# Kernel tuning notes

Hardware: AMD Instinct MI355X
Metric: run time of the kernel (lower is better)

## Reference

```python
import jax, jax.numpy as jnp
import numpy as np

_GAUSS_2D = np.array([[1.,4.,6.,4.,1.],[4.,16.,24.,16.,4.],[6.,24.,36.,24.,6.],[4.,16.,24.,16.,4.],[1.,4.,6.,4.,1.]], dtype=np.float32) / 256.0
_GX = np.array([[2.,0.,-2.],[4.,0.,-4.],[2.,0.,-2.]], dtype=np.float32)
_GY = np.array([[2.,4.,2.],[0.,0.,0.],[-2.,-4.,-2.]], dtype=np.float32)


def _conv_gauss(img, kernel):
    # reflect-pad by 2 on H,W (matches F.pad(img,(2,2,2,2),'reflect')), then depthwise VALID conv
    img = jnp.pad(img, ((0, 0), (0, 0), (2, 2), (2, 2)), mode='reflect')
    return jax.lax.conv_general_dilated(
        img, kernel, window_strides=(1, 1), padding='VALID',
        feature_group_count=img.shape[1],
        dimension_numbers=('NCHW', 'OIHW', 'NCHW'))


def _downsample(x):
    return x[:, :, ::2, ::2]


def _upsample(x, gk):
    # zero-interleave: x at even (h,w) indices, zeros elsewhere, then smooth with 4*gauss
    B, C, H, W = x.shape
    up = jnp.zeros((B, C, 2 * H, 2 * W), dtype=x.dtype).at[:, :, ::2, ::2].set(x)
    return _conv_gauss(up, 4.0 * gk)


def _laplacian_pyramid(img, gk, max_levels=3):
    C = img.shape[1]
    gx = jnp.broadcast_to(jnp.asarray(_GX)[None, None], (C, 1, 3, 3))
    gy = jnp.broadcast_to(jnp.asarray(_GY)[None, None], (C, 1, 3, 3))
    current = img
    pyr = []
    for _ in range(max_levels):
        filtered = _conv_gauss(current, gk)
        down = _downsample(filtered)
        up = _upsample(down, gk)
        diff = current - up
        # note: pad=2 with 3x3 kernel -> output is (H+2, W+2), faithful to source
        miniloss = jnp.abs(_conv_gauss(diff, gx)) + jnp.abs(_conv_gauss(diff, gy))
        pyr.append(miniloss)
        current = down
    return pyr


def setup_inputs() -> dict:
    key = jax.random.key(0)
    k1, k2 = jax.random.split(key)
    B, C, H, W = 16, 3, 512, 512
    inp = jax.random.normal(k1, (B, C, H, W), dtype=jnp.float32)
    tgt = jax.random.normal(k2, (B, C, H, W), dtype=jnp.float32)
    gk = jnp.broadcast_to(jnp.asarray(_GAUSS_2D)[None, None], (C, 1, 5, 5)).astype(jnp.float32)
    return {'input': inp, 'target': tgt, 'gauss_kernel': gk}


def reference(input, target, gauss_kernel):
    max_levels = 3
    pyr_in = _laplacian_pyramid(input, gauss_kernel, max_levels)
    pyr_tg = _laplacian_pyramid(target, gauss_kernel, max_levels)
    loss = jnp.asarray(0.0, dtype=input.dtype)
    for a, b in zip(pyr_in, pyr_tg):
        loss = loss + jnp.mean(jnp.abs(a - b))  # l1_loss, mean reduction
    return loss
```

## Files before the change

kernel.cpp:

```cpp
#include <hip/hip_runtime.h>


#define NCH 48

__device__ __forceinline__ int refl(int p, int n) {
  return p < 0 ? -p : (p >= n ? 2 * n - 2 - p : p);
}

__global__ __launch_bounds__(256) void down_kernel(
    const float* __restrict__ src_a, const float* __restrict__ src_b,
    float* __restrict__ dst_a, float* __restrict__ dst_b, int H)
{
  const int W = H, W2 = W >> 1;
  const int bx = blockIdx.x, by = blockIdx.y;
  const int z = blockIdx.z;
  const int ch = (z >= NCH) ? z - NCH : z;
  const float* src = ((z >= NCH) ? src_b : src_a) + (size_t)ch * H * W;
  float* dst = ((z >= NCH) ? dst_b : dst_a) + (size_t)ch * W2 * W2;
  const int tid = threadIdx.x;

  __shared__ __align__(16) float s_h[67][36];

  const int rb = 64 * by - 2;
  const int C0 = 64 * bx - 4;
  const bool lft = (bx == 0);
  const bool rgt = (64 * bx + 64 >= W);

  for (int t = tid; t < 67 * 18; t += 256) {
    int r = t / 18, c4 = t - 18 * r;
    int gr = refl(rb + r, H);
    int gb = min(max(C0 + 4 * c4, 0), W - 4);
    float4 v = *reinterpret_cast<const float4*>(src + (size_t)gr * W + gb);
    float pz = __shfl_up(v.z, 1);
    float pw = __shfl_up(v.w, 1);
    float nx = __shfl_down(v.x, 1);
    if (c4 >= 1 && c4 <= 16) {
      float hb0;
      if (lft && c4 == 1)
        hb0 = v.z + 4.f * v.y + 6.f * v.x + 4.f * v.y + v.z;
      else
        hb0 = pz + 4.f * pw + 6.f * v.x + 4.f * v.y + v.z;
      float nxe = (rgt && c4 == 16) ? v.z : nx;
      float hb1 = v.x + 4.f * v.y + 6.f * v.z + 4.f * v.w + nxe;
      *reinterpret_cast<float2*>(&s_h[r][2 * c4 - 2]) = make_float2(hb0, hb1);
    }
  }
  __syncthreads();

  {
    int r = tid >> 3, g = tid & 7;
    float4 h0 = *reinterpret_cast<const float4*>(&s_h[2 * r][4 * g]);
    float4 h1 = *reinterpret_cast<const float4*>(&s_h[2 * r + 1][4 * g]);
    float4 h2 = *reinterpret_cast<const float4*>(&s_h[2 * r + 2][4 * g]);
    float4 h3 = *reinterpret_cast<const float4*>(&s_h[2 * r + 3][4 * g]);
    float4 h4 = *reinterpret_cast<const float4*>(&s_h[2 * r + 4][4 * g]);
    float4 o;
    o.x = (h0.x + h4.x + 6.f * h2.x + 4.f * (h1.x + h3.x)) * (1.f / 256.f);
    o.y = (h0.y + h4.y + 6.f * h2.y + 4.f * (h1.y + h3.y)) * (1.f / 256.f);
    o.z = (h0.z + h4.z + 6.f * h2.z + 4.f * (h1.z + h3.z)) * (1.f / 256.f);
    o.w = (h0.w + h4.w + 6.f * h2.w + 4.f * (h1.w + h3.w)) * (1.f / 256.f);
    *reinterpret_cast<float4*>(dst + (size_t)(32 * by + r) * W2 + 32 * bx + 4 * g) = o;
  }
}

__global__ __launch_bounds__(256) void loss_kernel(
    const float* __restrict__ in, const float* __restrict__ tg,
    const float* __restrict__ d0i, const float* __restrict__ d0t,
    const float* __restrict__ d1i, const float* __restrict__ d1t,
    const float* __restrict__ d2i, const float* __restrict__ d2t,
    double* __restrict__ partials)
{
  int tb = blockIdx.x;
  int lvl, bx, by;
  if (tb < 289) { lvl = 0; by = tb / 17; bx = tb - 17 * by; }
  else if (tb < 370) { int u = tb - 289; lvl = 1; by = u / 9; bx = u - 9 * by; }
  else { int u = tb - 370; lvl = 2; by = u / 5; bx = u - 5 * by; }

  const int H = 512 >> lvl, W = H, HO = H + 2, H2 = H >> 1, W2 = W >> 1;
  const int n = blockIdx.z;
  const float* cb0 = (lvl == 0) ? in : (lvl == 1) ? d0i : d1i;
  const float* cb1 = (lvl == 0) ? tg : (lvl == 1) ? d0t : d1t;
  const float* db0 = (lvl == 0) ? d0i : (lvl == 1) ? d1i : d2i;
  const float* db1 = (lvl == 0) ? d0t : (lvl == 1) ? d1t : d2t;
  const float* curp[2] = {cb0 + (size_t)n * H * W, cb1 + (size_t)n * H * W};
  const float* dwp[2] = {db0 + (size_t)n * H2 * W2, db1 + (size_t)n * H2 * W2};
  const float scale = 1.f / (float)(NCH * HO * HO);

  const int x0 = bx * 32, y0 = by * 32;
  const int tid = threadIdx.x;

  __shared__ __align__(16) float s_diff[2][36][52];
  __shared__ __align__(16) float s_tmp[2][36][24];
  __shared__ __align__(16) float s_down[2][20][24];

  const bool fast = (x0 >= 12) && (x0 + 52 <= W) && (y0 >= 6) && (y0 + 37 <= H);

  const int y_end = min(HO, y0 + 32), x_end = min(HO, x0 + 32);
  int rlo = max(0, y0 - 2);
  if (y_end > H) rlo = min(rlo, 2 * H - 1 - y_end);
  int clo = max(0, x0 - 2);
  if (x_end > W) clo = min(clo, 2 * W - 1 - x_end);
  const int nrows = min(H, y_end) - rlo;
  const int ncols = min(W, x_end) - clo;

  const int dr0 = fast ? (y0 >> 1) - 2 : (max(0, rlo - 2) >> 1);
  const int du0 = fast ? (x0 >> 1) - 4 : (max(0, clo - 2) >> 1);

  if (fast) {
    const int cbase = x0 - 8;
    const int rbase = y0 - 2;
#pragma unroll
    for (int t = tid; t < 864; t += 256) {
      int img = t >= 432; int j = t - (img ? 432 : 0);
      int l = j / 12, c4 = j - 12 * l;
      *reinterpret_cast<float4*>(&s_diff[img][l][4 * c4]) =
          *reinterpret_cast<const float4*>(curp[img] + (size_t)(rbase + l) * W + cbase + 4 * c4);
    }
    if (tid < 240) {
      int img = tid >= 120; int j = tid - (img ? 120 : 0);
      int k = j / 6, c4 = j - 6 * k;
      *reinterpret_cast<float4*>(&s_down[img][k][4 * c4]) =
          *reinterpret_cast<const float4*>(dwp[img] + (size_t)(dr0 + k) * W2 + du0 + 4 * c4);
    }
  } else {
    for (int t = tid; t < 2448; t += 256) {
      int img = t >= 1224; int j = t - (img ? 1224 : 0);
      int l = j / 36, c = j - 36 * l;
      if (l < nrows && c < ncols)
        s_diff[img][l][c] = curp[img][(size_t)(rlo + l) * W + clo + c];
    }
    for (int t = tid; t < 960; t += 256) {
      int img = t >= 480; int j = t - (img ? 480 : 0);
      int k = j / 24, c = j - 24 * k;
      s_down[img][k][c] =
          dwp[img][(size_t)min(dr0 + k, H2 - 1) * W2 + min(du0 + c, W2 - 1)];
    }
  }
  __syncthreads();

  if (fast) {
    for (int t = tid; t < 432; t += 256) {
      int img = t / 216, j = t - 216 * img;
      int l = j / 6, c4 = j - 6 * l;
      int rr = (l + (l & 1)) >> 1;
      float4 a = *reinterpret_cast<const float4*>(&s_down[img][rr][4 * c4]);
      float4 b = *reinterpret_cast<const float4*>(&s_down[img][rr + 1][4 * c4]);
      float4 o;
      if (l & 1) {
        o.x = 0.5f * (a.x + b.x);
        o.y = 0.5f * (a.y + b.y);
        o.z = 0.5f * (a.z + b.z);
        o.w = 0.5f * (a.w + b.w);
      } else {
        float4 cc = *reinterpret_cast<const float4*>(&s_down[img][rr + 2][4 * c4]);
        o.x = 0.125f * (a.x + cc.x) + 0.75f * b.x;
        o.y = 0.125f * (a.y + cc.y) + 0.75f * b.y;
        o.z = 0.125f * (a.z + cc.z) + 0.75f * b.z;
        o.w = 0.125f * (a.w + cc.w) + 0.75f * b.w;
      }
      *reinterpret_cast<float4*>(&s_tmp[img][l][4 * c4]) = o;
    }
  } else {
    for (int t = tid; t < 2 * 34 * 24; t += 256) {
      int img = t / 816, j = t - 816 * img;
      int l = j / 24, du = j - 24 * l;
      int p = min(rlo + l, H - 1);
      int ur = min(du, W2 - 1 - du0);
      int par = p & 1;
      int f = p - 2 + par;
      int t0 = (refl(f, H) >> 1) - dr0;
      int t1 = (refl(f + 2, H) >> 1) - dr0;
      int t2 = (refl(f + 4, H) >> 1) - dr0;
      float w0v = par ? 0.5f : 0.125f;
      float w1v = par ? 0.5f : 0.75f;
      float w2v = par ? 0.0f : 0.125f;
      s_tmp[img][l][du] = w0v * s_down[img][t0][ur] + w1v * s_down[img][t1][ur]
                        + w2v * s_down[img][t2][ur];
    }
  }
  __syncthreads();

  if (fast) {
    for (int t = tid; t < 720; t += 256) {
      int img = t / 360, j = t - 360 * img;
      int l = j / 10, c4 = j - 10 * l;
      float4 c = *reinterpret_cast<const float4*>(&s_diff[img][l][4 * c4 + 4]);
      const float* st = s_tmp[img][l];
      float Tm1 = st[2 * c4 + 1], T0 = st[2 * c4 + 2], T1 = st[2 * c4 + 3], T2 = st[2 * c4 + 4];
      float4 d;
      d.x = c.x - (0.125f * (Tm1 + T1) + 0.75f * T0);
      d.y = c.y - 0.5f * (T0 + T1);
      d.z = c.z - (0.125f * (T0 + T2) + 0.75f * T1);
      d.w = c.w - 0.5f * (T1 + T2);
      *reinterpret_cast<float4*>(&s_diff[img][l][4 * c4 + 4]) = d;
    }
  } else {
    for (int t = tid; t < 2448; t += 256) {
      int img = t / 1224, j = t - 1224 * img;
      int l = j / 36, cc = j - 36 * l;
      if (l < nrows && cc < ncols) {
        int q = clo + cc;
        int par = q & 1;
        int f = q - 2 + par;
        int tA = (refl(f, W) >> 1) - du0;
        int tB = (refl(f + 2, W) >> 1) - du0;
        int tC = (refl(f + 4, W) >> 1) - du0;
        float w0v = par ? 0.5f : 0.125f;
        float w1v = par ? 0.5f : 0.75f;
        float w2v = par ? 0.0f : 0.125f;
        float up = w0v * s_tmp[img][l][tA] + w1v * s_tmp[img][l][tB]
                 + w2v * s_tmp[img][l][tC];
        s_diff[img][l][cc] -= up;
      }
    }
  }
  __syncthreads();

  float val = 0.f;
  if (fast) {
    const int tx = tid & 7, ty = tid >> 3;
    float ab[2][4];
#pragma unroll
    for (int img = 0; img < 2; ++img) {
      float a[3][6];
#pragma unroll
      for (int r = 0; r < 3; ++r) {
        const float* row = s_diff[img][ty + r];
        float4 M = *reinterpret_cast<const float4*>(&row[4 * tx + 4]);
        float4 R = *reinterpret_cast<const float4*>(&row[4 * tx + 8]);
        a[r][0] = M.z; a[r][1] = M.w; a[r][2] = R.x;
        a[r][3] = R.y; a[r][4] = R.z; a[r][5] = R.w;
      }
#pragma unroll
      for (int jj = 0; jj < 4; ++jj) {
        float tA = a[0][jj] - a[0][jj + 2];
        float tB = a[1][jj] - a[1][jj + 2];
        float tC = a[2][jj] - a[2][jj + 2];
        float gx = 2.f * (tA + tC) + 4.f * tB;
        float SA = 2.f * (a[0][jj] + a[0][jj + 2]) + 4.f * a[0][jj + 1];
        float SC = 2.f * (a[2][jj] + a[2][jj + 2]) + 4.f * a[2][jj + 1];
        ab[img][jj] = fabsf(gx) + fabsf(SA - SC);
      }
    }
#pragma unroll
    for (int jj = 0; jj < 4; ++jj) val += fabsf(ab[0][jj] - ab[1][jj]);
  } else {
    const int tx = tid & 31, tg8 = tid >> 5;
    const int xx = x0 + tx;
    if (xx < x_end) {
      const int cj0 = refl(xx - 2, W) - clo;
      const int cj1 = refl(xx - 1, W) - clo;
      const int cj2 = refl(xx, W) - clo;
      for (int k = 0; k < 4; ++k) {
        int yy = y0 + 4 * tg8 + k;
        if (yy >= y_end) break;
        int ri0 = refl(yy - 2, H) - rlo;
        int ri1 = refl(yy - 1, H) - rlo;
        int ri2 = refl(yy, H) - rlo;
        float ab2[2];
#pragma unroll
        for (int img = 0; img < 2; ++img) {
          float d00 = s_diff[img][ri0][cj0], d01 = s_diff[img][ri0][cj1], d02 = s_diff[img][ri0][cj2];
          float d10 = s_diff[img][ri1][cj0],                               d12 = s_diff[img][ri1][cj2];
          float d20 = s_diff[img][ri2][cj0], d21 = s_diff[img][ri2][cj1], d22 = s_diff[img][ri2][cj2];
          float gx = 2.f * (d00 - d02) + 4.f * (d10 - d12) + 2.f * (d20 - d22);
          float gy = 2.f * d00 + 4.f * d01 + 2.f * d02 - 2.f * d20 - 4.f * d21 - 2.f * d22;
          ab2[img] = fabsf(gx) + fabsf(gy);
        }
        val += fabsf(ab2[0] - ab2[1]);
      }
    }
  }
  val *= scale;

#pragma unroll
  for (int off = 32; off > 0; off >>= 1) val += __shfl_down(val, off, 64);
  __shared__ float wpart[4];
  if ((tid & 63) == 0) wpart[tid >> 6] = val;
  __syncthreads();
  if (tid == 0) {
    double s = (double)wpart[0] + (double)wpart[1] + (double)wpart[2] + (double)wpart[3];
    int lin = blockIdx.z * 395 + blockIdx.x;
    partials[lin] = s;
  }
}

__global__ __launch_bounds__(1024) void finalize_kernel(
    const double* __restrict__ partials, int N, float* __restrict__ out)
{
  double s = 0.0;
  for (int i = threadIdx.x; i < N; i += 1024) s += partials[i];
#pragma unroll
  for (int off = 32; off > 0; off >>= 1)
    s += __shfl_down(s, off, 64);
  __shared__ double wp[16];
  if ((threadIdx.x & 63) == 0) wp[threadIdx.x >> 6] = s;
  __syncthreads();
  if (threadIdx.x == 0) {
    double t = 0.0;
#pragma unroll
    for (int i = 0; i < 16; ++i) t += wp[i];
    out[0] = (float)t;
  }
}

extern "C" void kernel_launch(void* const* d_in, const int* in_sizes, int n_in,
                              void* d_out, int out_size, void* d_ws, size_t ws_size,
                              hipStream_t stream) {
  const float* in = (const float*)d_in[0];
  const float* tg = (const float*)d_in[1];
  float* out = (float*)d_out;

  const int NPART = 18960;
  double* partials = (double*)d_ws;
  float* base = (float*)((char*)d_ws + (size_t)NPART * sizeof(double));
  const size_t s0 = (size_t)NCH * 256 * 256;
  const size_t s1 = (size_t)NCH * 128 * 128;
  const size_t s2 = (size_t)NCH * 64 * 64;
  float* d0i = base;
  float* d0t = d0i + s0;
  float* d1i = d0t + s0;
  float* d1t = d1i + s1;
  float* d2i = d1t + s1;
  float* d2t = d2i + s2;

  down_kernel<<<dim3(8, 8, 2 * NCH), dim3(256), 0, stream>>>(in, tg, d0i, d0t, 512);
  down_kernel<<<dim3(4, 4, 2 * NCH), dim3(256), 0, stream>>>(d0i, d0t, d1i, d1t, 256);
  down_kernel<<<dim3(2, 2, 2 * NCH), dim3(256), 0, stream>>>(d1i, d1t, d2i, d2t, 128);

  loss_kernel<<<dim3(395, 1, NCH), dim3(256), 0, stream>>>(
      in, tg, d0i, d0t, d1i, d1t, d2i, d2t, partials);

  finalize_kernel<<<1, dim3(1024), 0, stream>>>(partials, NPART, out);
}
```

Baseline: 280.8 us.

## Fuse pyramid stages into one persistent cooperative kernel with grid syncs

Replaces the five separate launches (three downsample passes, loss, finalize) with one persistent cooperative kernel of 1280 blocks. It loops over tiles for each stage and separates the stages with grid-wide syncs. Shared memory is reused across stages, and s_diff shrinks from 52 to 48 columns so more blocks fit per CU. The aim is to remove launch gaps and the tail drain between kernels, at the cost of grid.sync overhead and fixed persistent-block scheduling. The old multi-kernel path stays as a fallback if the cooperative launch fails.

```diff
diff --git a/kernel.cpp b/kernel.cpp
--- a/kernel.cpp
+++ b/kernel.cpp
@@ -1,4 +1,7 @@
 #include <hip/hip_runtime.h>
+#include <hip/hip_cooperative_groups.h>
+
+namespace cg = cooperative_groups;
 
 
 #define NCH 48
@@ -7,20 +10,11 @@
   return p < 0 ? -p : (p >= n ? 2 * n - 2 - p : p);
 }
 
-__global__ __launch_bounds__(256) void down_kernel(
-    const float* __restrict__ src_a, const float* __restrict__ src_b,
-    float* __restrict__ dst_a, float* __restrict__ dst_b, int H)
+__device__ __forceinline__ void down_tile(
+    const float* __restrict__ src, float* __restrict__ dst,
+    int H, int bx, int by, float (*s_h)[36], int tid)
 {
   const int W = H, W2 = W >> 1;
-  const int bx = blockIdx.x, by = blockIdx.y;
-  const int z = blockIdx.z;
-  const int ch = (z >= NCH) ? z - NCH : z;
-  const float* src = ((z >= NCH) ? src_b : src_a) + (size_t)ch * H * W;
-  float* dst = ((z >= NCH) ? dst_b : dst_a) + (size_t)ch * W2 * W2;
-  const int tid = threadIdx.x;
-
-  __shared__ __align__(16) float s_h[67][36];
-
   const int rb = 64 * by - 2;
   const int C0 = 64 * bx - 4;
   const bool lft = (bx == 0);
@@ -61,37 +55,22 @@
     o.w = (h0.w + h4.w + 6.f * h2.w + 4.f * (h1.w + h3.w)) * (1.f / 256.f);
     *reinterpret_cast<float4*>(dst + (size_t)(32 * by + r) * W2 + 32 * bx + 4 * g) = o;
   }
-}
-
-__global__ __launch_bounds__(256) void loss_kernel(
-    const float* __restrict__ in, const float* __restrict__ tg,
-    const float* __restrict__ d0i, const float* __restrict__ d0t,
-    const float* __restrict__ d1i, const float* __restrict__ d1t,
-    const float* __restrict__ d2i, const float* __restrict__ d2t,
-    double* __restrict__ partials)
-{
-  int tb = blockIdx.x;
-  int lvl, bx, by;
-  if (tb < 289) { lvl = 0; by = tb / 17; bx = tb - 17 * by; }
-  else if (tb < 370) { int u = tb - 289; lvl = 1; by = u / 9; bx = u - 9 * by; }
-  else { int u = tb - 370; lvl = 2; by = u / 5; bx = u - 5 * by; }
-
-  const int H = 512 >> lvl, W = H, HO = H + 2, H2 = H >> 1, W2 = W >> 1;
-  const int n = blockIdx.z;
-  const float* cb0 = (lvl == 0) ? in : (lvl == 1) ? d0i : d1i;
-  const float* cb1 = (lvl == 0) ? tg : (lvl == 1) ? d0t : d1t;
-  const float* db0 = (lvl == 0) ? d0i : (lvl == 1) ? d1i : d2i;
-  const float* db1 = (lvl == 0) ? d0t : (lvl == 1) ? d1t : d2t;
-  const float* curp[2] = {cb0 + (size_t)n * H * W, cb1 + (size_t)n * H * W};
-  const float* dwp[2] = {db0 + (size_t)n * H2 * W2, db1 + (size_t)n * H2 * W2};
+  __syncthreads();
+}
+
+__device__ __forceinline__ double loss_tile(
+    const float* __restrict__ cur0, const float* __restrict__ cur1,
+    const float* __restrict__ dw0, const float* __restrict__ dw1,
+    int H, int bx, int by,
+    float (*s_diff)[36][48], float (*s_tmp)[36][24], float (*s_down)[20][24],
+    float* wpart, int tid)
+{
+  const int W = H, HO = H + 2, H2 = H >> 1, W2 = W >> 1;
+  const float* curp[2] = {cur0, cur1};
+  const float* dwp[2] = {dw0, dw1};
   const float scale = 1.f / (float)(NCH * HO * HO);
 
   const int x0 = bx * 32, y0 = by * 32;
-  const int tid = threadIdx.x;
-
-  __shared__ __align__(16) float s_diff[2][36][52];
-  __shared__ __align__(16) float s_tmp[2][36][24];
-  __shared__ __align__(16) float s_down[2][20][24];
 
   const bool fast = (x0 >= 12) && (x0 + 52 <= W) && (y0 >= 6) && (y0 + 37 <= H);
 
@@ -275,14 +254,137 @@
 
 #pragma unroll
   for (int off = 32; off > 0; off >>= 1) val += __shfl_down(val, off, 64);
+  if ((tid & 63) == 0) wpart[tid >> 6] = val;
+  __syncthreads();
+  double s = 0.0;
+  if (tid == 0)
+    s = (double)wpart[0] + (double)wpart[1] + (double)wpart[2] + (double)wpart[3];
+  return s;
+}
+
+__global__ __launch_bounds__(256, 5) void fused_all(
+    const float* __restrict__ in, const float* __restrict__ tg,
+    float* __restrict__ d0i, float* __restrict__ d0t,
+    float* __restrict__ d1i, float* __restrict__ d1t,
+    float* __restrict__ d2i, float* __restrict__ d2t,
+    double* __restrict__ partials, float* __restrict__ out)
+{
+  cg::grid_group grid = cg::this_grid();
+  const int tid = threadIdx.x;
+  const int bid = blockIdx.x;
+  const int nblk = gridDim.x;
+
+  __shared__ __align__(16) float smem[6144];
   __shared__ float wpart[4];
-  if ((tid & 63) == 0) wpart[tid >> 6] = val;
-  __syncthreads();
-  if (tid == 0) {
-    double s = (double)wpart[0] + (double)wpart[1] + (double)wpart[2] + (double)wpart[3];
-    int lin = blockIdx.z * 395 + blockIdx.x;
-    partials[lin] = s;
-  }
+  __shared__ double wpd[4];
+  float (*s_h)[36] = reinterpret_cast<float (*)[36]>(smem);
+  float (*s_diff)[36][48] = reinterpret_cast<float (*)[36][48]>(smem);
+  float (*s_tmp)[36][24] = reinterpret_cast<float (*)[36][24]>(smem + 3456);
+  float (*s_down)[20][24] = reinterpret_cast<float (*)[20][24]>(smem + 5184);
+
+  for (int u = bid; u < 6144; u += nblk) {
+    int z = u >> 6, rm = u & 63, by = rm >> 3, bx = rm & 7;
+    int ch = (z >= NCH) ? z - NCH : z;
+    const float* src = ((z >= NCH) ? tg : in) + (size_t)ch * 512 * 512;
+    float* dst = ((z >= NCH) ? d0t : d0i) + (size_t)ch * 256 * 256;
+    down_tile(src, dst, 512, bx, by, s_h, tid);
+  }
+  __threadfence();
+  grid.sync();
+
+  for (int u = bid; u < 1536; u += nblk) {
+    int z = u >> 4, rm = u & 15, by = rm >> 2, bx = rm & 3;
+    int ch = (z >= NCH) ? z - NCH : z;
+    const float* src = ((z >= NCH) ? d0t : d0i) + (size_t)ch * 256 * 256;
+    float* dst = ((z >= NCH) ? d1t : d1i) + (size_t)ch * 128 * 128;
+    down_tile(src, dst, 256, bx, by, s_h, tid);
+  }
+  __threadfence();
+  grid.sync();
+
+  for (int u = bid; u < 384; u += nblk) {
+    int z = u >> 2, rm = u & 3, by = rm >> 1, bx = rm & 1;
+    int ch = (z >= NCH) ? z - NCH : z;
+    const float* src = ((z >= NCH) ? d1t : d1i) + (size_t)ch * 128 * 128;
+    float* dst = ((z >= NCH) ? d2t : d2i) + (size_t)ch * 64 * 64;
+    down_tile(src, dst, 128, bx, by, s_h, tid);
+  }
+  __threadfence();
+  grid.sync();
+
+  for (int u = bid; u < 18960; u += nblk) {
+    int z = u / 395, tb = u - 395 * z;
+    int lvl, bx, by;
+    if (tb < 289) { lvl = 0; by = tb / 17; bx = tb - 17 * by; }
+    else if (tb < 370) { int q = tb - 289; lvl = 1; by = q / 9; bx = q - 9 * by; }
+    else { int q = tb - 370; lvl = 2; by = q / 5; bx = q - 5 * by; }
+    const int H = 512 >> lvl;
+    const float* cb0 = (lvl == 0) ? in : (lvl == 1) ? d0i : d1i;
+    const float* cb1 = (lvl == 0) ? tg : (lvl == 1) ? d0t : d1t;
+    const float* db0 = (lvl == 0) ? d0i : (lvl == 1) ? d1i : d2i;
+    const float* db1 = (lvl == 0) ? d0t : (lvl == 1) ? d1t : d2t;
+    size_t co = (size_t)z * H * H;
+    size_t dof = (size_t)z * (H >> 1) * (H >> 1);
+    double s = loss_tile(cb0 + co, cb1 + co, db0 + dof, db1 + dof,
+                         H, bx, by, s_diff, s_tmp, s_down, wpart, tid);
+    if (tid == 0) partials[u] = s;
+    __syncthreads();
+  }
+  __threadfence();
+  grid.sync();
+
+  if (bid == 0) {
+    double s = 0.0;
+    for (int i = tid; i < 18960; i += 256) s += partials[i];
+#pragma unroll
+    for (int off = 32; off > 0; off >>= 1) s += __shfl_down(s, off, 64);
+    if ((tid & 63) == 0) wpd[tid >> 6] = s;
+    __syncthreads();
+    if (tid == 0) out[0] = (float)(wpd[0] + wpd[1] + wpd[2] + wpd[3]);
+  }
+}
+
+__global__ __launch_bounds__(256) void down_kernel(
+    const float* __restrict__ src_a, const float* __restrict__ src_b,
+    float* __restrict__ dst_a, float* __restrict__ dst_b, int H)
+{
+  const int W = H, W2 = W >> 1;
+  const int bx = blockIdx.x, by = blockIdx.y;
+  const int z = blockIdx.z;
+  const int ch = (z >= NCH) ? z - NCH : z;
+  const float* src = ((z >= NCH) ? src_b : src_a) + (size_t)ch * H * W;
+  float* dst = ((z >= NCH) ? dst_b : dst_a) + (size_t)ch * W2 * W2;
+  __shared__ __align__(16) float s_h[67][36];
+  down_tile(src, dst, H, bx, by, s_h, threadIdx.x);
+}
+
+__global__ __launch_bounds__(256) void loss_kernel(
+    const float* __restrict__ in, const float* __restrict__ tg,
+    const float* __restrict__ d0i, const float* __restrict__ d0t,
+    const float* __restrict__ d1i, const float* __restrict__ d1t,
+    const float* __restrict__ d2i, const float* __restrict__ d2t,
+    double* __restrict__ partials)
+{
+  int tb = blockIdx.x;
+  int lvl, bx, by;
+  if (tb < 289) { lvl = 0; by = tb / 17; bx = tb - 17 * by; }
+  else if (tb < 370) { int u = tb - 289; lvl = 1; by = u / 9; bx = u - 9 * by; }
+  else { int u = tb - 370; lvl = 2; by = u / 5; bx = u - 5 * by; }
+  const int H = 512 >> lvl;
+  const int n = blockIdx.z;
+  const float* cb0 = (lvl == 0) ? in : (lvl == 1) ? d0i : d1i;
+  const float* cb1 = (lvl == 0) ? tg : (lvl == 1) ? d0t : d1t;
+  const float* db0 = (lvl == 0) ? d0i : (lvl == 1) ? d1i : d2i;
+  const float* db1 = (lvl == 0) ? d0t : (lvl == 1) ? d1t : d2t;
+  size_t co = (size_t)n * H * H;
+  size_t dof = (size_t)n * (H >> 1) * (H >> 1);
+  __shared__ __align__(16) float s_diff[2][36][48];
+  __shared__ __align__(16) float s_tmp[2][36][24];
+  __shared__ __align__(16) float s_down[2][20][24];
+  __shared__ float wpart[4];
+  double s = loss_tile(cb0 + co, cb1 + co, db0 + dof, db1 + dof,
+                       H, bx, by, s_diff, s_tmp, s_down, wpart, threadIdx.x);
+  if (threadIdx.x == 0) partials[blockIdx.z * 395 + blockIdx.x] = s;
 }
 
 __global__ __launch_bounds__(1024) void finalize_kernel(
@@ -324,12 +426,23 @@
   float* d2i = d1t + s1;
   float* d2t = d2i + s2;
 
+  static bool coop_ok = true;
+  if (coop_ok) {
+    const float* a0 = in; const float* a1 = tg;
+    float* p0 = d0i; float* p1 = d0t; float* p2 = d1i; float* p3 = d1t;
+    float* p4 = d2i; float* p5 = d2t;
+    double* pp = partials; float* po = out;
+    void* args[] = {&a0, &a1, &p0, &p1, &p2, &p3, &p4, &p5, &pp, &po};
+    hipError_t e = hipLaunchCooperativeKernel(
+        (const void*)fused_all, dim3(1280), dim3(256), args, 0, stream);
+    if (e == hipSuccess) return;
+    coop_ok = false;
+  }
+
   down_kernel<<<dim3(8, 8, 2 * NCH), dim3(256), 0, stream>>>(in, tg, d0i, d0t, 512);
   down_kernel<<<dim3(4, 4, 2 * NCH), dim3(256), 0, stream>>>(d0i, d0t, d1i, d1t, 256);
   down_kernel<<<dim3(2, 2, 2 * NCH), dim3(256), 0, stream>>>(d1i, d1t, d2i, d2t, 128);
-
   loss_kernel<<<dim3(395, 1, NCH), dim3(256), 0, stream>>>(
       in, tg, d0i, d0t, d1i, d1t, d2i, d2t, partials);
-
   finalize_kernel<<<1, dim3(1024), 0, stream>>>(partials, NPART, out);
 }
```

New measurement: 279.3 us. Within noise of the previous version (-0.5%).
